# Kernel optimization log

Hardware: AMD Instinct MI355X
Metric: run time of the kernel (lower is better)

Reference implementation:

```python
import jax, jax.numpy as jnp
import numpy as np

DIM = 1024
IMG_H, IMG_W = 512, 1408
CROP = 224
IMAGE_ORDER = (2, 0, 1, 5, 3, 4)
B, NC, NB = 2, 6, 32


def setup_inputs():
    key = jax.random.key(0)
    ks = jax.random.split(key, 12)
    camera_imgs = jax.random.normal(ks[0], (B, NC, 3, IMG_H, IMG_W), jnp.float32)
    u = jax.random.uniform(ks[1], (B, NB, 9), dtype=jnp.float32)
    centers = jnp.stack([u[..., 0] * 45.0 + 5.0,
                         (u[..., 1] - 0.5) * 40.0,
                         (u[..., 2] - 0.5) * 4.0], -1)
    pred_boxes = jnp.concatenate([centers, u[..., 3:] * 2.0], -1)  # [B,NB,9]
    K = np.array([[500., 0., IMG_W / 2.], [0., 500., IMG_H / 2.], [0., 0., 1.]])
    R_l2c = np.array([[0., -1., 0.], [0., 0., -1.], [1., 0., 0.]])  # lidar->camera axes
    mats = np.zeros((NC, 4, 4), np.float32)
    for c in range(NC):
        yaw = 2.0 * np.pi * c / NC
        Rz = np.array([[np.cos(yaw), -np.sin(yaw), 0.], [np.sin(yaw), np.cos(yaw), 0.], [0., 0., 1.]])
        mats[c, :3, :3] = K @ R_l2c @ Rz.T
        mats[c, 3, 3] = 1.0
    lidar2image = jnp.broadcast_to(jnp.asarray(mats), (B, NC, 4, 4))
    eye4 = jnp.eye(4, dtype=jnp.float32)
    img_aug_matrix = jnp.broadcast_to(eye4, (B, NC, 4, 4))
    lidar_aug_matrix = jnp.broadcast_to(eye4, (B, 4, 4))
    momentum = jnp.float32(0.5)
    box_default_dim = jax.random.normal(ks[2], (1, DIM), jnp.float32)
    theta_w = jnp.zeros((4, 9), jnp.float32)  # zero-init as in torch code
    theta_b = jnp.array([1., 0., 0., 1.], jnp.float32)

    def cw(k, shape):
        fan = shape[1] * shape[2] * shape[3]
        return jax.random.normal(k, shape, jnp.float32) * (2.0 / fan) ** 0.5
    conv1 = cw(ks[3], (64, 3, 7, 7))
    conv2 = cw(ks[4], (256, 64, 3, 3))
    conv3 = cw(ks[5], (DIM, 256, 3, 3))
    pos_embed = jax.random.normal(ks[6], (50, DIM), jnp.float32) * 0.02
    s = DIM ** -0.5
    wq = jax.random.normal(ks[7], (DIM, DIM), jnp.float32) * s
    wk = jax.random.normal(ks[8], (DIM, DIM), jnp.float32) * s
    wv = jax.random.normal(ks[9], (DIM, DIM), jnp.float32) * s
    wo = jax.random.normal(ks[10], (DIM, DIM), jnp.float32) * s
    return dict(camera_imgs=camera_imgs, pred_boxes=pred_boxes,
                img_aug_matrix=img_aug_matrix, lidar_aug_matrix=lidar_aug_matrix,
                lidar2image=lidar2image, momentum=momentum,
                box_default_dim=box_default_dim, theta_w=theta_w, theta_b=theta_b,
                conv1=conv1, conv2=conv2, conv3=conv3, pos_embed=pos_embed,
                wq=wq, wk=wk, wv=wv, wo=wo)


def _project(pred_boxes, lidar_aug_matrix, lidar2image, img_aug_matrix):
    # returns vu [B,NC,NB,2] = (row, col) pixel coords, on_img [B,NC,NB]
    def per_b(boxes, la, l2i, aug):
        c = boxes[:, :3] - la[:3, 3]                       # [NB,3]
        c = jnp.linalg.inv(la[:3, :3]) @ c.T               # [3,NB]
        c = l2i[:, :3, :3] @ c + l2i[:, :3, 3:4]           # [NC,3,NB]
        z = jnp.clip(c[:, 2], 1e-5, 1e5)
        xy = c[:, :2] / z[:, None]
        c = jnp.concatenate([xy, z[:, None]], 1)
        c = aug[:, :3, :3] @ c + aug[:, :3, 3:4]
        uv = c[:, :2].transpose(0, 2, 1)                   # [NC,NB,2] (col,row)
        vu = uv[..., ::-1]                                 # (row,col)
        on = (vu[..., 0] < IMG_H) & (vu[..., 0] >= 0) & (vu[..., 1] < IMG_W) & (vu[..., 1] >= 0)
        return vu, on
    return jax.vmap(per_b)(pred_boxes, lidar_aug_matrix, lidar2image, img_aug_matrix)


def _base_grid(h, w):
    # torch affine_grid align_corners=False pixel-center coords
    xs = (2.0 * jnp.arange(w) + 1.0) / w - 1.0
    ys = (2.0 * jnp.arange(h) + 1.0) / h - 1.0
    gx, gy = jnp.meshgrid(xs, ys)  # [h,w]
    return jnp.stack([gx, gy, jnp.ones_like(gx)], -1)  # [h,w,3]


def _grid_sample(img, grid):
    # img [C,H,W]; grid [...,2] xy in [-1,1]; bilinear, zeros padding, align_corners=False
    C, H, W = img.shape
    ix = ((grid[..., 0] + 1.0) * W - 1.0) / 2.0
    iy = ((grid[..., 1] + 1.0) * H - 1.0) / 2.0
    x0 = jnp.floor(ix); y0 = jnp.floor(iy)
    x1 = x0 + 1.0; y1 = y0 + 1.0
    wx = ix - x0; wy = iy - y0

    def gather(xx, yy):
        xi = jnp.clip(xx, 0, W - 1).astype(jnp.int32)
        yi = jnp.clip(yy, 0, H - 1).astype(jnp.int32)
        valid = (xx >= 0) & (xx <= W - 1) & (yy >= 0) & (yy <= H - 1)
        return img[:, yi, xi] * valid.astype(img.dtype)  # [C, ...]
    v00 = gather(x0, y0); v01 = gather(x1, y0)
    v10 = gather(x0, y1); v11 = gather(x1, y1)
    return (v00 * (1 - wx) * (1 - wy) + v01 * wx * (1 - wy)
            + v10 * (1 - wx) * wy + v11 * wx * wy)  # [C, ...]


def _clip_head(x, conv1, conv2, conv3, pos_embed, wq, wk, wv, wo):
    dn = ('NCHW', 'OIHW', 'NCHW')
    h = jax.nn.relu(jax.lax.conv_general_dilated(x, conv1, (4, 4), 'SAME', dimension_numbers=dn))
    h = jax.nn.relu(jax.lax.conv_general_dilated(h, conv2, (4, 4), 'SAME', dimension_numbers=dn))
    h = jax.nn.relu(jax.lax.conv_general_dilated(h, conv3, (2, 2), 'SAME', dimension_numbers=dn))  # [M,D,7,7]
    tok = h.reshape(h.shape[0], DIM, 49).transpose(0, 2, 1)              # [M,49,D]
    tok = jnp.concatenate([tok.mean(1, keepdims=True), tok], 1) + pos_embed  # [M,50,D]
    q = tok[:, :1] @ wq
    k = tok @ wk
    v = tok @ wv
    attn = jax.nn.softmax((q @ k.transpose(0, 2, 1)) * (DIM ** -0.5), -1)
    return ((attn @ v) @ wo)[:, 0]  # [M,D]


def reference(camera_imgs, pred_boxes, img_aug_matrix, lidar_aug_matrix, lidar2image,
              momentum, box_default_dim, theta_w, theta_b,
              conv1, conv2, conv3, pos_embed, wq, wk, wv, wo):
    N = B * NB
    vu, on_img = _project(pred_boxes, lidar_aug_matrix, lidar2image, img_aug_matrix)  # [B,NC,NB,2],[B,NC,NB]
    boxes_flat = pred_boxes.reshape(N, 9)
    rot = jnp.tanh(boxes_flat @ theta_w.T + theta_b).reshape(N, 2, 2)   # theta_rot MLP
    ty = vu[..., 0] / IMG_H * 2.0 - 1.0                                 # [B,NC,NB]
    tx = vu[..., 1] / IMG_W * 2.0 - 1.0
    pos = jnp.stack([tx, ty], -1).transpose(0, 2, 1, 3).reshape(N, NC, 2)
    theta = jnp.concatenate([jnp.broadcast_to(rot[:, None], (N, NC, 2, 2)),
                             pos[..., None]], -1)                        # [N,NC,2,3]
    base = _base_grid(CROP, CROP)                                        # [224,224,3]
    grids = jnp.einsum('hwk,ncjk->nchwj', base, theta)                   # [N,NC,224,224,2]
    grids = grids.reshape(B, NB, NC, CROP, CROP, 2)
    crops = []
    for b in range(B):
        for c in range(NC):
            smp = _grid_sample(camera_imgs[b, c], grids[b, :, c])        # [3,NB,224,224]
            crops.append(smp.transpose(1, 0, 2, 3))
    crops = jnp.stack(crops).reshape(B, NC, NB, 3, CROP, CROP)
    crops = crops.transpose(0, 2, 1, 3, 4, 5).reshape(N * NC, 3, CROP, CROP)
    emb = _clip_head(crops, conv1, conv2, conv3, pos_embed, wq, wk, wv, wo).reshape(N, NC, DIM)
    valid = on_img.transpose(0, 2, 1).reshape(N, NC)
    e = jnp.broadcast_to(box_default_dim, (N, DIM))
    for c in IMAGE_ORDER:  # sequential EMA over cameras, skipping off-image ones
        m = valid[:, c:c + 1]
        e = jnp.where(m, momentum * e + (1.0 - momentum) * emb[:, c], e)
    return e  # [N, DIM]
```

## Files before the change

kernel.cpp:

```cpp
#include <hip/hip_runtime.h>
#include <hip/hip_bf16.h>

#define DIMN 1024
#define IMG_H 512
#define IMG_W 1408
#define CROPN 224
#define NCAM 6
#define NBOXB 32
#define NBOX 64
#define NIMG 384

typedef __hip_bfloat16 bf16;
typedef unsigned short u16;
typedef float f32x4 __attribute__((ext_vector_type(4)));
typedef short bf16x8 __attribute__((ext_vector_type(8)));
typedef u16 u16x4 __attribute__((ext_vector_type(4)));
typedef u16 u16x8 __attribute__((ext_vector_type(8)));

__device__ __forceinline__ float b2f(bf16 x) { return __bfloat162float(x); }
__device__ __forceinline__ u16 f2us(float x) {
  bf16 h = __float2bfloat16(x);
  return *(u16*)&h;
}
__device__ __forceinline__ bf16x8 as_b(u16x8 x) {
  union { u16x8 u; bf16x8 b; } c; c.u = x; return c.b;
}

__global__ void k_w1r(const float* __restrict__ in, u16* __restrict__ out) {
  int idx = blockIdx.x * 256 + threadIdx.x;
  if (idx >= 64 * 224) return;
  int oc = idx / 224, t = idx % 224;
  int r = t >> 5, u = t & 31, kw = u >> 2, ch = u & 3;
  u16 v = (kw < 7 && ch < 3) ? f2us(in[((oc * 3 + ch) * 7 + r) * 7 + kw]) : (u16)0;
  out[(((oc >> 4) * 28 + (t >> 3)) * 16 + (oc & 15)) * 8 + (t & 7)] = v;
}
__global__ void k_w2r(const float* __restrict__ in, u16* __restrict__ out) {
  int idx = blockIdx.x * 256 + threadIdx.x;
  if (idx >= 256 * 576) return;
  int oc = idx / 576, t = idx % 576;
  int rk = t >> 6, ic = t & 63, r = rk / 3, kw = rk % 3;
  u16 v = f2us(in[((oc * 64 + ic) * 3 + r) * 3 + kw]);
  out[(((oc >> 4) * 72 + (t >> 3)) * 16 + (oc & 15)) * 8 + (t & 7)] = v;
}
__global__ void k_w3r(const float* __restrict__ in, u16* __restrict__ out) {
  int idx = blockIdx.x * 256 + threadIdx.x;
  if (idx >= 1024 * 2304) return;
  int oc = idx / 2304, t = idx % 2304;
  int rk = t >> 8, ic = t & 255, r = rk / 3, kw = rk % 3;
  u16 v = f2us(in[((oc * 256 + ic) * 3 + r) * 3 + kw]);
  int ocb = oc >> 4, mm = oc & 15, kb = t >> 3, kj = t & 7;
  out[(((size_t)ocb * 288 + kb) * 16 + mm) * 8 + kj] = v;
}
__global__ void k_transpose_t(const float* __restrict__ w, float* __restrict__ wt) {
  __shared__ float tile[32][33];
  int x = blockIdx.x * 32 + threadIdx.x;
  for (int j = threadIdx.y; j < 32; j += 8)
    tile[j][threadIdx.x] = w[(size_t)(blockIdx.y * 32 + j) * 1024 + x];
  __syncthreads();
  int x2 = blockIdx.y * 32 + threadIdx.x;
  for (int j = threadIdx.y; j < 32; j += 8)
    wt[(size_t)(blockIdx.x * 32 + j) * 1024 + x2] = tile[threadIdx.x][j];
}

__global__ void k_proj(const float* __restrict__ boxes, const float* __restrict__ la_m,
                       const float* __restrict__ l2i, const float* __restrict__ aug,
                       const float* __restrict__ tw, const float* __restrict__ tb,
                       float* __restrict__ theta_out, int* __restrict__ valid_out) {
  int t = threadIdx.x;
  if (t >= NIMG) return;
  int n = t / NCAM, cam = t % NCAM;
  int b = n / NBOXB, nb = n % NBOXB;

  float la[4][4];
  for (int r = 0; r < 4; r++)
    for (int c = 0; c < 4; c++) la[r][c] = la_m[b * 16 + r * 4 + c];
  float a00=la[0][0],a01=la[0][1],a02=la[0][2];
  float a10=la[1][0],a11=la[1][1],a12=la[1][2];
  float a20=la[2][0],a21=la[2][1],a22=la[2][2];
  float c00 =  a11*a22 - a12*a21;
  float c01 = -(a10*a22 - a12*a20);
  float c02 =  a10*a21 - a11*a20;
  float det = a00*c00 + a01*c01 + a02*c02;
  float id = 1.0f / det;
  float inv[3][3];
  inv[0][0] = c00*id;                 inv[0][1] = -(a01*a22-a02*a21)*id;  inv[0][2] =  (a01*a12-a02*a11)*id;
  inv[1][0] = c01*id;                 inv[1][1] =  (a00*a22-a02*a20)*id;  inv[1][2] = -(a00*a12-a02*a10)*id;
  inv[2][0] = c02*id;                 inv[2][1] = -(a00*a21-a01*a20)*id;  inv[2][2] =  (a00*a11-a01*a10)*id;

  float bx[9];
  for (int i = 0; i < 9; i++) bx[i] = boxes[(b * NBOXB + nb) * 9 + i];
  float c0[3] = { bx[0]-la[0][3], bx[1]-la[1][3], bx[2]-la[2][3] };
  float c1[3];
  for (int r = 0; r < 3; r++) c1[r] = inv[r][0]*c0[0] + inv[r][1]*c0[1] + inv[r][2]*c0[2];

  const float* M = l2i + (size_t)(b * NCAM + cam) * 16;
  float p[3];
  for (int r = 0; r < 3; r++)
    p[r] = M[r*4+0]*c1[0] + M[r*4+1]*c1[1] + M[r*4+2]*c1[2] + M[r*4+3];
  float z = fminf(fmaxf(p[2], 1e-5f), 100000.0f);
  float x = p[0] / z, y = p[1] / z;
  const float* A = aug + (size_t)(b * NCAM + cam) * 16;
  float u = A[0]*x + A[1]*y + A[2]*z + A[3];
  float v = A[4]*x + A[5]*y + A[6]*z + A[7];

  int on = (v < (float)IMG_H) && (v >= 0.0f) && (u < (float)IMG_W) && (u >= 0.0f);
  float ty = v / (float)IMG_H * 2.0f - 1.0f;
  float tx = u / (float)IMG_W * 2.0f - 1.0f;

  float s[4];
  for (int j = 0; j < 4; j++) {
    float acc = tb[j];
    for (int i = 0; i < 9; i++) acc += tw[j * 9 + i] * bx[i];
    s[j] = tanhf(acc);
  }
  float* o = theta_out + t * 6;
  o[0] = s[0]; o[1] = s[1]; o[2] = tx;
  o[3] = s[2]; o[4] = s[3]; o[5] = ty;
  valid_out[t] = on;
}

#define HALO_PX 1356
__global__ void k_zero_halo(u16x4* __restrict__ c) {
  int t = blockIdx.x * 256 + threadIdx.x;
  int i = t / HALO_PX;
  if (i >= NIMG) return;
  int r = t % HALO_PX;
  int ph, pw;
  if (r < 684) {
    int rr = r / 228;
    ph = (rr == 0) ? 0 : (rr == 1 ? 225 : 226);
    pw = r % 228;
  } else {
    int q = r - 684;
    ph = 1 + q / 3;
    int s = q % 3;
    pw = (s == 0) ? 0 : (s == 1 ? 225 : 226);
  }
  c[(size_t)i * 228 * 228 + ph * 228 + pw] = (u16x4){0, 0, 0, 0};
}

__global__ __launch_bounds__(256) void k_sample(const float* __restrict__ imgs,
                                                const float* __restrict__ theta,
                                                u16* __restrict__ crops) {
  int idx = blockIdx.x * 256 + threadIdx.x;
  int i = idx / (CROPN * CROPN);
  int rem = idx - i * (CROPN * CROPN);
  int yy = rem / CROPN, xx = rem % CROPN;
  const float* th = theta + i * 6;
  float gx = (2.0f * xx + 1.0f) / (float)CROPN - 1.0f;
  float gy = (2.0f * yy + 1.0f) / (float)CROPN - 1.0f;
  float grid_x = th[0]*gx + th[1]*gy + th[2];
  float grid_y = th[3]*gx + th[4]*gy + th[5];
  float ix = ((grid_x + 1.0f) * (float)IMG_W - 1.0f) * 0.5f;
  float iy = ((grid_y + 1.0f) * (float)IMG_H - 1.0f) * 0.5f;
  float x0 = floorf(ix), y0 = floorf(iy);
  float wx = ix - x0, wy = iy - y0;
  int cam = i % NCAM, b = i / (NBOXB * NCAM);
  const float* base = imgs + (size_t)(b * NCAM + cam) * 3 * IMG_H * IMG_W;

  float xf[2] = { x0, x0 + 1.0f };
  float yf[2] = { y0, y0 + 1.0f };
  float wxa[2] = { 1.0f - wx, wx };
  float wya[2] = { 1.0f - wy, wy };
  int   xi[2], yi[2], vx[2], vy[2];
  for (int j = 0; j < 2; j++) {
    vx[j] = (xf[j] >= 0.0f) && (xf[j] <= (float)(IMG_W - 1));
    vy[j] = (yf[j] >= 0.0f) && (yf[j] <= (float)(IMG_H - 1));
    xi[j] = (int)fminf(fmaxf(xf[j], 0.0f), (float)(IMG_W - 1));
    yi[j] = (int)fminf(fmaxf(yf[j], 0.0f), (float)(IMG_H - 1));
  }
  float res[3];
  #pragma unroll
  for (int ch = 0; ch < 3; ch++) {
    const float* cp = base + (size_t)ch * IMG_H * IMG_W;
    float r = 0.0f;
    #pragma unroll
    for (int jy = 0; jy < 2; jy++)
      #pragma unroll
      for (int jx = 0; jx < 2; jx++) {
        float val = (vx[jx] && vy[jy]) ? cp[yi[jy] * IMG_W + xi[jx]] : 0.0f;
        r += val * wxa[jx] * wya[jy];
      }
    res[ch] = r;
  }
  u16x4 st = { f2us(res[0]), f2us(res[1]), f2us(res[2]), 0 };
  *(u16x4*)(crops + ((size_t)i * 228 * 228 + (size_t)(yy + 1) * 228 + (xx + 1)) * 4) = st;
}


#define C1_GROUPS 34
__global__ __launch_bounds__(256) void k_conv1m(const u16* __restrict__ X,
                                                const u16* __restrict__ W,
                                                u16* __restrict__ out) {
  __shared__ u16x8 sX[C1_GROUPS * 64];
  int blk = blockIdx.x;
  int i = blk / 14, rg = blk % 14;
  int tid = threadIdx.x, wv = tid >> 6, lane = tid & 63;
  int m = lane & 15, quad = lane >> 4;

  const u16* src = X + ((size_t)i * 51984 + (size_t)(rg * 16) * 228) * 4;
  #pragma unroll
  for (int j = 0; j < 9; j++) {
    int g = wv + j * 4;
    if (g < C1_GROUPS) {
      int c = g * 64 + lane;
      int cc = c < 2166 ? c : 2165;
      __builtin_amdgcn_global_load_lds(
          (const __attribute__((address_space(1))) void*)(src + (size_t)cc * 8),
          (__attribute__((address_space(3))) void*)(sX + g * 64),
          16, 0, 0);
    }
  }
  __syncthreads();

  int col[4];
  #pragma unroll
  for (int nt = 0; nt < 4; nt++) col[nt] = nt * 16 + m;
  f32x4 acc[4][4];
  #pragma unroll
  for (int t = 0; t < 4; t++)
    #pragma unroll
    for (int nt = 0; nt < 4; nt++) acc[t][nt] = (f32x4){0.f, 0.f, 0.f, 0.f};

  #pragma unroll
  for (int r = 0; r < 7; r++) {
    bf16x8 a[4];
    #pragma unroll
    for (int t = 0; t < 4; t++)
      a[t] = as_b(*(const u16x8*)(W + (size_t)(((t * 28 + r * 4 + quad) * 16 + m) * 8)));
    int lrow = wv * 4 + r;
    #pragma unroll
    for (int nt = 0; nt < 4; nt++) {
      int cl = col[nt] < 56 ? col[nt] : 55;
      bf16x8 bfr = as_b(sX[lrow * 114 + cl * 2 + quad]);
      #pragma unroll
      for (int t = 0; t < 4; t++)
        acc[t][nt] = __builtin_amdgcn_mfma_f32_16x16x32_bf16(a[t], bfr, acc[t][nt], 0, 0, 0);
    }
  }
  int oh = rg * 4 + wv;
  #pragma unroll
  for (int nt = 0; nt < 4; nt++) {
    if (col[nt] < 56) {
      int n = oh * 56 + col[nt];
      #pragma unroll
      for (int t = 0; t < 4; t++) {
        u16x4 st;
        #pragma unroll
        for (int r4 = 0; r4 < 4; r4++) st[r4] = f2us(fmaxf(acc[t][nt][r4], 0.f));
        *(u16x4*)(out + ((size_t)i * 3136 + n) * 64 + t * 16 + quad * 4) = st;
      }
    }
  }
}

__global__ __launch_bounds__(256, 3) void k_conv2m(const u16* __restrict__ X,
                                                   const u16* __restrict__ W,
                                                   u16* __restrict__ out) {
  __shared__ u16x8 s2[3136];
  int bid = blockIdx.x;
  int i = bid / 7, ohg = bid % 7;
  int tid = threadIdx.x, wv = tid >> 6, lane = tid & 63;
  int m = lane & 15, quad = lane >> 4;

  const u16* src = X + ((size_t)i * 3136 + 8 * ohg * 56) * 64;
  u16x8 tmp[13];
  #pragma unroll
  for (int j = 0; j < 13; j++) {
    int c = tid + j * 256;
    int cc = c < 3136 ? c : 3135;
    tmp[j] = *(const u16x8*)(src + (size_t)cc * 8);
  }
  #pragma unroll
  for (int j = 0; j < 13; j++) {
    int c = tid + j * 256;
    int cc = c < 3136 ? c : 3135;
    int pixel = cc >> 3;
    int li = pixel / 56, iw = pixel - li * 56;
    int g = (14 * (li >> 2) + (iw >> 2)) & 15;
    s2[(cc & ~15) | ((cc ^ g) & 15)] = tmp[j];
  }
  __syncthreads();

  int nl[2], pk2[9][2];
  #pragma unroll
  for (int nt = 0; nt < 2; nt++) {
    int n = nt * 16 + m;
    nl[nt] = n;
    int nc = n < 28 ? n : 27;
    int ohl = nc / 14, ow = nc - ohl * 14;
    int g = nc & 15;
    #pragma unroll
    for (int rk = 0; rk < 9; rk++) {
      int r = rk / 3, kw = rk % 3;
      int pixel = (ohl * 4 + r) * 56 + (ow * 4 + kw);
      int cb = pixel * 8;
      int base2 = (cb & ~15) | ((cb & 8) ^ (g & 8));
      pk2[rk][nt] = base2 | (g & 7);
    }
  }
  f32x4 acc[4][2];
  #pragma unroll
  for (int t = 0; t < 4; t++)
    #pragma unroll
    for (int nt = 0; nt < 2; nt++) acc[t][nt] = (f32x4){0.f, 0.f, 0.f, 0.f};

  const u16* wbase = W + (size_t)(wv * 4) * (72 * 128) + m * 8;
  auto loadA = [&](int t, int s) {
    return as_b(*(const u16x8*)(wbase + (size_t)(t * 72 + s * 4 + quad) * 128));
  };
  auto loadB = [&](int nt, int s) {
    int pkv = pk2[s >> 1][nt];
    int sub = (s & 1) * 4 + quad;
    return as_b(s2[(pkv & ~7) | (sub ^ (pkv & 7))]);
  };

  bf16x8 A_[3][4], B_[3][2];
  #pragma unroll
  for (int t = 0; t < 4; t++) { A_[0][t] = loadA(t, 0); A_[1][t] = loadA(t, 1); }
  #pragma unroll
  for (int nt = 0; nt < 2; nt++) { B_[0][nt] = loadB(nt, 0); B_[1][nt] = loadB(nt, 1); }

  #pragma unroll
  for (int s = 0; s < 18; s++) {
    if (s + 2 < 18) {
      #pragma unroll
      for (int t = 0; t < 4; t++) A_[(s + 2) % 3][t] = loadA(t, s + 2);
      #pragma unroll
      for (int nt = 0; nt < 2; nt++) B_[(s + 2) % 3][nt] = loadB(nt, s + 2);
    }
    #pragma unroll
    for (int nt = 0; nt < 2; nt++)
      #pragma unroll
      for (int t = 0; t < 4; t++)
        acc[t][nt] = __builtin_amdgcn_mfma_f32_16x16x32_bf16(A_[s % 3][t], B_[s % 3][nt], acc[t][nt], 0, 0, 0);
  }

  #pragma unroll
  for (int nt = 0; nt < 2; nt++) {
    if (nl[nt] < 28) {
      int n = ohg * 28 + nl[nt];
      #pragma unroll
      for (int t = 0; t < 4; t++) {
        u16x4 st;
        #pragma unroll
        for (int r4 = 0; r4 < 4; r4++) st[r4] = f2us(fmaxf(acc[t][nt][r4], 0.f));
        *(u16x4*)(out + ((size_t)i * 196 + n) * 256 + wv * 64 + t * 16 + quad * 4) = st;
      }
    }
  }
}

__global__ __launch_bounds__(512, 2) void k_conv3m(const u16* __restrict__ X,
                                                   const u16* __restrict__ W,
                                                   float* __restrict__ out3) {
  __shared__ u16x8 sX8[6688];
  int bid = blockIdx.x;
  int og = (bid >> 2) & 1;
  int i  = (bid >> 3) * 4 + (bid & 3);
  int tid = threadIdx.x;

  const u16* src = X + (size_t)i * (196 * 256);
  u16x8 tmp[13];
  #pragma unroll
  for (int j = 0; j < 13; j++) {
    int c = tid + j * 512;
    int cc = c < 6272 ? c : 6271;
    tmp[j] = *(const u16x8*)(src + (size_t)cc * 8);
  }
  #pragma unroll
  for (int j = 0; j < 13; j++) {
    int c = tid + j * 512;
    int p = c >> 5;
    int ih = p / 14, iw = p - ih * 14;
    int g = (7 * (ih >> 1) + (iw >> 1)) & 15;
    sX8[(c & ~15) | ((c ^ g) & 15)] = tmp[j];
  }
  if (tid < 32) sX8[6656 + tid] = (u16x8){0,0,0,0,0,0,0,0};
  __syncthreads();

  int wv = tid >> 6, lane = tid & 63;
  int m = lane & 15, quad = lane >> 4;
  int ocw = og * 512 + wv * 64;
  int narr[4], oh2[4], ow2[4];
  #pragma unroll
  for (int nt = 0; nt < 4; nt++) {
    int n = nt * 16 + m;
    narr[nt] = n;
    int nc = n < 49 ? n : 48;
    int oh = nc / 7, ow = nc - oh * 7;
    oh2[nt] = oh * 2; ow2[nt] = ow * 2;
  }
  int pk[9][4];
  #pragma unroll
  for (int rk = 0; rk < 9; rk++) {
    int r = rk / 3, kw = rk % 3;
    #pragma unroll
    for (int nt = 0; nt < 4; nt++) {
      int ih = oh2[nt] + r, iw = ow2[nt] + kw;
      bool valid = (narr[nt] < 49) && (ih < 14) && (iw < 14);
      int p = ih * 14 + iw;
      int g = (7 * (ih >> 1) + (iw >> 1)) & 15;
      pk[rk][nt] = valid ? (((p * 32) << 4) | g) : (6656 << 4);
    }
  }
  f32x4 acc[4][4];
  #pragma unroll
  for (int t = 0; t < 4; t++)
    #pragma unroll
    for (int nt = 0; nt < 4; nt++) acc[t][nt] = (f32x4){0.f, 0.f, 0.f, 0.f};

  const u16* wbase = W + (size_t)(ocw >> 4) * (288 * 128) + m * 8;

  auto loadA = [&](int t, int s) {
    return as_b(*(const u16x8*)(wbase + (size_t)(t * 288 + 4 * s + quad) * 128));
  };
  auto loadB = [&](int nt, int s) {
    int pkv = pk[s >> 3][nt];
    int q = (s & 7) * 4 + quad;
    return as_b(sX8[(pkv >> 4) + (q ^ (pkv & 15))]);
  };

  bf16x8 A_[3][4], B_[3][4];
  #pragma unroll
  for (int t = 0; t < 4; t++) { A_[0][t] = loadA(t, 0); A_[1][t] = loadA(t, 1); }
  #pragma unroll
  for (int nt = 0; nt < 4; nt++) { B_[0][nt] = loadB(nt, 0); B_[1][nt] = loadB(nt, 1); }

  #pragma unroll
  for (int s = 0; s < 72; s++) {
    if (s + 2 < 72) {
      #pragma unroll
      for (int t = 0; t < 4; t++) A_[(s + 2) % 3][t] = loadA(t, s + 2);
      #pragma unroll
      for (int nt = 0; nt < 4; nt++) B_[(s + 2) % 3][nt] = loadB(nt, s + 2);
    }
    #pragma unroll
    for (int nt = 0; nt < 4; nt++)
      #pragma unroll
      for (int t = 0; t < 4; t++)
        acc[t][nt] = __builtin_amdgcn_mfma_f32_16x16x32_bf16(A_[s % 3][t], B_[s % 3][nt], acc[t][nt], 0, 0, 0);
  }

  #pragma unroll
  for (int nt = 0; nt < 4; nt++) {
    int n = narr[nt];
    if (n < 49) {
      #pragma unroll
      for (int t = 0; t < 4; t++) {
        f32x4 o;
        #pragma unroll
        for (int r4 = 0; r4 < 4; r4++) o[r4] = fmaxf(acc[t][nt][r4], 0.f);
        *(f32x4*)(out3 + ((size_t)i * 49 + n) * DIMN + ocw + t * 16 + quad * 4) = o;
      }
    }
  }
}

__global__ __launch_bounds__(256) void k_tok(const float* __restrict__ h,
                                             const float* __restrict__ pos,
                                             float* __restrict__ tok) {
  int blk = blockIdx.x;
  int i = blk / 50, t = blk % 50;
  int d = threadIdx.x * 4;
  float4 val;
  if (t == 0) {
    float sx = 0, sy = 0, sz = 0, sw = 0;
    for (int p = 0; p < 49; p++) {
      float4 v = *(const float4*)(h + ((size_t)i * 49 + p) * DIMN + d);
      sx += v.x; sy += v.y; sz += v.z; sw += v.w;
    }
    const float inv49 = 1.0f / 49.0f;
    val.x = sx * inv49; val.y = sy * inv49; val.z = sz * inv49; val.w = sw * inv49;
  } else {
    val = *(const float4*)(h + ((size_t)i * 49 + (t - 1)) * DIMN + d);
  }
  float4 pe = *(const float4*)(pos + (size_t)t * DIMN + d);
  float4 o; o.x = val.x + pe.x; o.y = val.y + pe.y; o.z = val.z + pe.z; o.w = val.w + pe.w;
  *(float4*)(tok + ((size_t)i * 50 + t) * DIMN + d) = o;
}

__global__ __launch_bounds__(256) void k_matvec2(const float* __restrict__ vecs, int vstride,
                                                 const float* __restrict__ M,
                                                 float* __restrict__ out) {
  __shared__ float s_v[4][DIMN];
  int i0 = blockIdx.x * 4;
  int h = blockIdx.y;
  for (int e = threadIdx.x; e < 4 * DIMN; e += 256)
    s_v[e >> 10][e & 1023] = vecs[(size_t)(i0 + (e >> 10)) * vstride + (e & 1023)];
  __syncthreads();
  int d0 = h * 512 + threadIdx.x * 2;
  float2 acc[4] = {{0,0},{0,0},{0,0},{0,0}};
  for (int e = 0; e < DIMN; e++) {
    float2 w = *(const float2*)(M + (size_t)e * DIMN + d0);
    #pragma unroll
    for (int im = 0; im < 4; im++) {
      float x = s_v[im][e];
      acc[im].x += x * w.x; acc[im].y += x * w.y;
    }
  }
  #pragma unroll
  for (int im = 0; im < 4; im++)
    *(float2*)(out + (size_t)(i0 + im) * DIMN + d0) = acc[im];
}

__global__ __launch_bounds__(256) void k_attn(const float* __restrict__ tok,
                                              const float* __restrict__ a1,
                                              float* __restrict__ tvec) {
  __shared__ float s_a[DIMN];
  __shared__ float s_sc[50];
  __shared__ float s_at[50];
  int i = blockIdx.x;
  for (int e = threadIdx.x; e < DIMN; e += 256) s_a[e] = a1[(size_t)i * DIMN + e];
  __syncthreads();
  int wave = threadIdx.x >> 6, lane = threadIdx.x & 63;
  for (int t = wave; t < 50; t += 4) {
    const float* tr = tok + ((size_t)i * 50 + t) * DIMN;
    float p = 0.0f;
    for (int mm = 0; mm < 16; mm++) {
      int e = lane + mm * 64;
      p += tr[e] * s_a[e];
    }
    for (int off = 32; off > 0; off >>= 1) p += __shfl_down(p, off, 64);
    if (lane == 0) s_sc[t] = p * 0.03125f;
  }
  __syncthreads();
  if (threadIdx.x == 0) {
    float mx = s_sc[0];
    for (int t = 1; t < 50; t++) mx = fmaxf(mx, s_sc[t]);
    float sum = 0.0f;
    for (int t = 0; t < 50; t++) { float ex = expf(s_sc[t] - mx); s_at[t] = ex; sum += ex; }
    float inv = 1.0f / sum;
    for (int t = 0; t < 50; t++) s_at[t] *= inv;
  }
  __syncthreads();
  int d0 = threadIdx.x * 4;
  float ax = 0, ay = 0, az = 0, aw = 0;
  for (int t = 0; t < 50; t++) {
    float at = s_at[t];
    float4 tv = *(const float4*)(tok + ((size_t)i * 50 + t) * DIMN + d0);
    ax += at * tv.x; ay += at * tv.y; az += at * tv.z; aw += at * tv.w;
  }
  float4 o; o.x = ax; o.y = ay; o.z = az; o.w = aw;
  *(float4*)(tvec + (size_t)i * DIMN + d0) = o;
}

__global__ void k_final(const float* __restrict__ emb,
                        const int* __restrict__ valid,
                        const float* __restrict__ bdd,
                        const float* __restrict__ momp,
                        float* __restrict__ out) {
  int n = blockIdx.x;
  int d0 = threadIdx.x * 4;
  float mom = momp[0];
  float e[4];
  #pragma unroll
  for (int j = 0; j < 4; j++) e[j] = bdd[d0 + j];
  const int order[6] = {2, 0, 1, 5, 3, 4};
  #pragma unroll
  for (int s = 0; s < 6; s++) {
    int c = order[s];
    int i = n * NCAM + c;
    if (valid[i]) {
      const float* er = emb + (size_t)i * DIMN + d0;
      #pragma unroll
      for (int j = 0; j < 4; j++) e[j] = mom * e[j] + (1.0f - mom) * er[j];
    }
  }
  #pragma unroll
  for (int j = 0; j < 4; j++) out[(size_t)n * DIMN + d0 + j] = e[j];
}

extern "C" void kernel_launch(void* const* d_in, const int* in_sizes, int n_in,
                              void* d_out, int out_size, void* d_ws, size_t ws_size,
                              hipStream_t stream) {
  const float* in_cam = (const float*)d_in[0];
  const float* in_box = (const float*)d_in[1];
  const float* in_aug = (const float*)d_in[2];
  const float* in_la  = (const float*)d_in[3];
  const float* in_l2i = (const float*)d_in[4];
  const float* in_mom = (const float*)d_in[5];
  const float* in_bdd = (const float*)d_in[6];
  const float* in_tw  = (const float*)d_in[7];
  const float* in_tb  = (const float*)d_in[8];
  const float* in_c1  = (const float*)d_in[9];
  const float* in_c2  = (const float*)d_in[10];
  const float* in_c3  = (const float*)d_in[11];
  const float* in_pe  = (const float*)d_in[12];
  const float* in_wq  = (const float*)d_in[13];
  const float* in_wk  = (const float*)d_in[14];
  const float* in_wv  = (const float*)d_in[15];
  const float* in_wo  = (const float*)d_in[16];

  char* base = (char*)d_ws;
  size_t off = 0;
  auto carve = [&](size_t bytes) -> char* {
    char* p = base + off;
    off += (bytes + 255) & ~(size_t)255;
    return p;
  };
  float* theta   = (float*)carve((size_t)NIMG * 6 * 4);
  int*   valid   = (int*)carve((size_t)NIMG * 4);
  float* qbuf    = (float*)carve((size_t)NIMG * DIMN * 4);
  float* a1buf   = (float*)carve((size_t)NIMG * DIMN * 4);
  float* tvbuf   = (float*)carve((size_t)NIMG * DIMN * 4);
  float* ctxbuf  = (float*)carve((size_t)NIMG * DIMN * 4);
  float* embbuf  = (float*)carve((size_t)NIMG * DIMN * 4);
  float* wkT_f   = (float*)carve((size_t)DIMN * DIMN * 4);
  u16*   W1r     = (u16*)carve((size_t)64 * 224 * 2);
  u16*   W2r     = (u16*)carve((size_t)256 * 576 * 2);
  u16*   W3r     = (u16*)carve((size_t)1024 * 2304 * 2);
  u16*   c2o     = (u16*)carve((size_t)NIMG * 196 * 256 * 2);
  char*  R1      = carve((size_t)NIMG * 228 * 228 * 4 * 2);
  u16*   c1o     = (u16*)carve((size_t)NIMG * 3136 * 64 * 2);
  u16*   crops   = (u16*)R1;
  float* conv3o  = (float*)R1;
  float* tok     = (float*)(R1 + (size_t)NIMG * 49 * DIMN * 4);

  k_w1r<<<56, 256, 0, stream>>>(in_c1, W1r);
  k_w2r<<<576, 256, 0, stream>>>(in_c2, W2r);
  k_w3r<<<9216, 256, 0, stream>>>(in_c3, W3r);
  k_transpose_t<<<dim3(32, 32), dim3(32, 8), 0, stream>>>(in_wk, wkT_f);

  k_proj<<<1, 384, 0, stream>>>(in_box, in_la, in_l2i, in_aug, in_tw, in_tb, theta, valid);
  k_zero_halo<<<(NIMG * HALO_PX + 255) / 256, 256, 0, stream>>>((u16x4*)crops);
  k_sample<<<(NIMG * CROPN * CROPN) / 256, 256, 0, stream>>>(in_cam, theta, crops);
  k_conv1m<<<NIMG * 14, 256, 0, stream>>>(crops, W1r, c1o);
  k_conv2m<<<NIMG * 7, 256, 0, stream>>>(c1o, W2r, c2o);
  k_conv3m<<<768, 512, 0, stream>>>(c2o, W3r, conv3o);
  k_tok<<<NIMG * 50, 256, 0, stream>>>(conv3o, in_pe, tok);
  k_matvec2<<<dim3(96, 2), 256, 0, stream>>>(tok, 50 * DIMN, in_wq, qbuf);
  k_matvec2<<<dim3(96, 2), 256, 0, stream>>>(qbuf, DIMN, wkT_f, a1buf);
  k_attn<<<NIMG, 256, 0, stream>>>(tok, a1buf, tvbuf);
  k_matvec2<<<dim3(96, 2), 256, 0, stream>>>(tvbuf, DIMN, in_wv, ctxbuf);
  k_matvec2<<<dim3(96, 2), 256, 0, stream>>>(ctxbuf, DIMN, in_wo, embbuf);
  k_final<<<NBOX, 256, 0, stream>>>(embbuf, valid, in_bdd, in_mom, (float*)d_out);
}
```

Before: 951.7 us.

## Load conv3 input tile via direct global-to-LDS and cut register pressure

Swaps the register-staged global->LDS copy of the conv3 input tile for __builtin_amdgcn_global_load_lds, which writes straight into shared memory. The XOR swizzle moves to the global-side address because each wave writes a contiguous 64-slot block. It also drops the precomputed 9x4 pk offset table in favour of per-kernel-row offsets recomputed every 8 steps, and shrinks B prefetch from triple to double buffering. Together these cut VGPR use and staging instructions, at the cost of shorter B prefetch distance and more index math inside the loop.

```diff
diff --git a/kernel.cpp b/kernel.cpp
--- a/kernel.cpp
+++ b/kernel.cpp
@@ -359,27 +359,27 @@
   int og = (bid >> 2) & 1;
   int i  = (bid >> 3) * 4 + (bid & 3);
   int tid = threadIdx.x;
+  int wv = tid >> 6, lane = tid & 63;
 
   const u16* src = X + (size_t)i * (196 * 256);
-  u16x8 tmp[13];
   #pragma unroll
   for (int j = 0; j < 13; j++) {
-    int c = tid + j * 512;
-    int cc = c < 6272 ? c : 6271;
-    tmp[j] = *(const u16x8*)(src + (size_t)cc * 8);
-  }
-  #pragma unroll
-  for (int j = 0; j < 13; j++) {
-    int c = tid + j * 512;
-    int p = c >> 5;
-    int ih = p / 14, iw = p - ih * 14;
-    int g = (7 * (ih >> 1) + (iw >> 1)) & 15;
-    sX8[(c & ~15) | ((c ^ g) & 15)] = tmp[j];
+    int gi = (j < 12) ? (wv + j * 8) : (96 + wv);
+    if (j < 12 || wv < 2) {
+      int slot = gi * 64 + lane;
+      int p = slot >> 5;
+      int ih = p / 14, iw = p - ih * 14;
+      int g = (7 * (ih >> 1) + (iw >> 1)) & 15;
+      int c = (slot & ~15) | ((slot ^ g) & 15);
+      __builtin_amdgcn_global_load_lds(
+          (const __attribute__((address_space(1))) void*)(src + (size_t)c * 8),
+          (__attribute__((address_space(3))) void*)(sX8 + gi * 64),
+          16, 0, 0);
+    }
   }
   if (tid < 32) sX8[6656 + tid] = (u16x8){0,0,0,0,0,0,0,0};
   __syncthreads();
 
-  int wv = tid >> 6, lane = tid & 63;
   int m = lane & 15, quad = lane >> 4;
   int ocw = og * 512 + wv * 64;
   int narr[4], oh2[4], ow2[4];
@@ -391,55 +391,59 @@
     int oh = nc / 7, ow = nc - oh * 7;
     oh2[nt] = oh * 2; ow2[nt] = ow * 2;
   }
-  int pk[9][4];
-  #pragma unroll
-  for (int rk = 0; rk < 9; rk++) {
-    int r = rk / 3, kw = rk % 3;
+  f32x4 acc[4][4];
+  #pragma unroll
+  for (int t = 0; t < 4; t++)
+    #pragma unroll
+    for (int nt = 0; nt < 4; nt++) acc[t][nt] = (f32x4){0.f, 0.f, 0.f, 0.f};
+
+  const u16* wbase = W + (size_t)(ocw >> 4) * (288 * 128) + m * 8;
+
+  int bc[4], bk[4];
+  auto set_bparams = [&](int rk) {
+    const int r = rk / 3, kw = rk % 3;
     #pragma unroll
     for (int nt = 0; nt < 4; nt++) {
       int ih = oh2[nt] + r, iw = ow2[nt] + kw;
       bool valid = (narr[nt] < 49) && (ih < 14) && (iw < 14);
       int p = ih * 14 + iw;
-      int g = (7 * (ih >> 1) + (iw >> 1)) & 15;
-      pk[rk][nt] = valid ? (((p * 32) << 4) | g) : (6656 << 4);
-    }
-  }
-  f32x4 acc[4][4];
-  #pragma unroll
-  for (int t = 0; t < 4; t++)
-    #pragma unroll
-    for (int nt = 0; nt < 4; nt++) acc[t][nt] = (f32x4){0.f, 0.f, 0.f, 0.f};
-
-  const u16* wbase = W + (size_t)(ocw >> 4) * (288 * 128) + m * 8;
-
+      bc[nt] = valid ? p * 32 : 6656;
+      bk[nt] = valid ? ((7 * (ih >> 1) + (iw >> 1)) & 15) : 0;
+    }
+  };
   auto loadA = [&](int t, int s) {
     return as_b(*(const u16x8*)(wbase + (size_t)(t * 288 + 4 * s + quad) * 128));
   };
-  auto loadB = [&](int nt, int s) {
-    int pkv = pk[s >> 3][nt];
-    int q = (s & 7) * 4 + quad;
-    return as_b(sX8[(pkv >> 4) + (q ^ (pkv & 15))]);
+  auto loadB = [&](int nt, int q4) {
+    return as_b(sX8[bc[nt] + ((q4 + quad) ^ bk[nt])]);
   };
 
-  bf16x8 A_[3][4], B_[3][4];
-  #pragma unroll
-  for (int t = 0; t < 4; t++) { A_[0][t] = loadA(t, 0); A_[1][t] = loadA(t, 1); }
-  #pragma unroll
-  for (int nt = 0; nt < 4; nt++) { B_[0][nt] = loadB(nt, 0); B_[1][nt] = loadB(nt, 1); }
+  bf16x8 A_[3][4], B_[2][4];
+  set_bparams(0);
+  #pragma unroll
+  for (int t = 0; t < 4; t++) {
+    A_[0][t] = loadA(t, 0);
+    A_[1][t] = loadA(t, 1);
+  }
+  #pragma unroll
+  for (int nt = 0; nt < 4; nt++) B_[0][nt] = loadB(nt, 0);
 
   #pragma unroll
   for (int s = 0; s < 72; s++) {
     if (s + 2 < 72) {
       #pragma unroll
       for (int t = 0; t < 4; t++) A_[(s + 2) % 3][t] = loadA(t, s + 2);
-      #pragma unroll
-      for (int nt = 0; nt < 4; nt++) B_[(s + 2) % 3][nt] = loadB(nt, s + 2);
+    }
+    if (s + 1 < 72) {
+      if (((s + 1) & 7) == 0) set_bparams((s + 1) >> 3);
+      #pragma unroll
+      for (int nt = 0; nt < 4; nt++) B_[(s + 1) & 1][nt] = loadB(nt, ((s + 1) & 7) * 4);
     }
     #pragma unroll
     for (int nt = 0; nt < 4; nt++)
       #pragma unroll
       for (int t = 0; t < 4; t++)
-        acc[t][nt] = __builtin_amdgcn_mfma_f32_16x16x32_bf16(A_[s % 3][t], B_[s % 3][nt], acc[t][nt], 0, 0, 0);
+        acc[t][nt] = __builtin_amdgcn_mfma_f32_16x16x32_bf16(A_[s % 3][t], B_[s & 1][nt], acc[t][nt], 0, 0, 0);
   }
 
   #pragma unroll
```

After: 937.4 us. About the same (-1.5%).
